# Kernel tuning notes

Hardware: AMD Instinct MI355X
Metric: run time of the kernel (lower is better)

## Reference

```python
import jax, jax.numpy as jnp
import numpy as np

B, T, C = 2, 2048, 1024
H, GAMMA = 16, 8
D = C // H
SCALE = 1.0 / np.sqrt(D).astype(np.float32)


def setup_inputs() -> dict:
    key = jax.random.key(0)
    ks = jax.random.split(key, 6)
    w = 0.02
    return {
        'x': jax.random.normal(ks[0], (B, T, C), dtype=jnp.float32),
        'Wq': jax.random.normal(ks[1], (C, 2 * C), dtype=jnp.float32) * w,
        'Wk': jax.random.normal(ks[2], (C, 2 * C), dtype=jnp.float32) * w,
        'Wv': jax.random.normal(ks[3], (C, C), dtype=jnp.float32) * w,
        'Wo': jax.random.normal(ks[4], (C, C), dtype=jnp.float32) * w,
        'theta_offset': jax.random.normal(ks[5], (H,), dtype=jnp.float32) * 0.1,
    }


def _heads(t):
    # (B, T, C) -> (B, H, T, D)
    return t.reshape(B, T, H, D).transpose(0, 2, 1, 3)


def reference(x, Wq, Wk, Wv, Wo, theta_offset):
    q_raw = x @ Wq                      # (B, T, 2C)
    k_raw = x @ Wk                      # (B, T, 2C)
    v = _heads(x @ Wv)                  # (B, H, T, D)

    q_amp, q_phase = jnp.split(q_raw, 2, axis=-1)
    k_amp, k_phase = jnp.split(k_raw, 2, axis=-1)
    q_amp = jax.nn.softplus(_heads(q_amp))
    q_phase = _heads(q_phase)
    k_amp = jax.nn.softplus(_heads(k_amp))
    k_phase = _heads(k_phase)

    q_real = q_amp * jnp.cos(q_phase)
    q_imag = q_amp * jnp.sin(q_phase)
    k_real = k_amp * jnp.cos(k_phase)
    k_imag = k_amp * jnp.sin(k_phase)

    scores = (jnp.einsum('bhtd,bhsd->bhts', q_real, k_real)
              + jnp.einsum('bhtd,bhsd->bhts', q_imag, k_imag)) * SCALE

    # theta gating (active since T > GAMMA)
    cycle_ids = jnp.arange(T, dtype=jnp.float32) / GAMMA
    cycle_dist = cycle_ids[None, :] - cycle_ids[:, None]        # (T, T)
    theta_gate = jnp.cos(theta_offset[:, None, None] * cycle_dist)  # (H, T, T)
    scores = scores * theta_gate[None]

    causal = jnp.tril(jnp.ones((T, T), dtype=bool))
    scores = jnp.where(causal[None, None], scores, -jnp.inf)
    attn = jax.nn.softmax(scores, axis=-1)

    out = jnp.einsum('bhts,bhsd->bhtd', attn, v)
    out = out.transpose(0, 2, 1, 3).reshape(B, T, C)
    return out @ Wo
```

## Files before the change

### kernel.cpp

```cpp
#include <hip/hip_runtime.h>
#include <hip/hip_bf16.h>
#include <math.h>

#define Bc 2
#define Tc 2048
#define Cc 1024
#define Hc 16
#define Dc 64

typedef __attribute__((ext_vector_type(8))) short short8;
typedef __attribute__((ext_vector_type(4))) float f32x4;

#define L2E 1.44269504088896f
#define SM_M 20.0f

__device__ __forceinline__ short f2bf(float x) {
    unsigned u = __float_as_uint(x);
    u += 0x7fff + ((u >> 16) & 1);
    return (short)(u >> 16);
}
__device__ __forceinline__ unsigned pack2bf_fast(float a, float b) {
    unsigned ua = __float_as_uint(a) + 0x8000u;
    unsigned ub = __float_as_uint(b) + 0x8000u;
    return __builtin_amdgcn_perm(ub, ua, 0x07060302);
}
__device__ __forceinline__ float softplus_fast(float a) {
    return fmaxf(a, 0.f) + __logf(1.f + __expf(-fabsf(a)));
}

template <int EPI>
__global__ __launch_bounds__(256) void gemm_bt_mfma(
    const short* __restrict__ A, const short* __restrict__ Bt,
    float* __restrict__ Cf, short* __restrict__ Cb, short* __restrict__ Cb2,
    int M, int N, int K)
{
    __shared__ __attribute__((aligned(16))) short As[128 * 32];
    __shared__ __attribute__((aligned(16))) short Bs[128 * 32];

    const int tid = threadIdx.x;
    const int wave = tid >> 6, lane = tid & 63;
    const int quad = lane >> 4, c = lane & 15;
    const int wm = wave >> 1, wn = wave & 1;
    const int m0 = blockIdx.y * 128, n0 = blockIdx.x * 128;

    const int srow = lane >> 2;
    const int scol = (lane & 3) * 8;
    const short* Ag = A  + (size_t)(m0 + wave * 32 + srow) * K + scol;
    const short* Bg = Bt + (size_t)(n0 + wave * 32 + srow) * K + scol;
    short* AsW = As + (wave * 32) * 32;
    short* BsW = Bs + (wave * 32) * 32;

    f32x4 acc[4][4];
#pragma unroll
    for (int i = 0; i < 4; ++i)
#pragma unroll
        for (int j = 0; j < 4; ++j)
            acc[i][j] = (f32x4){0.f, 0.f, 0.f, 0.f};

    for (int k0 = 0; k0 < K; k0 += 32) {
        __syncthreads();
#pragma unroll
        for (int i = 0; i < 2; ++i) {
            __builtin_amdgcn_global_load_lds(
                (const __attribute__((address_space(1))) void*)(Ag + k0 + (size_t)i * 16 * K),
                (__attribute__((address_space(3))) void*)(AsW + i * 16 * 32), 16, 0, 0);
            __builtin_amdgcn_global_load_lds(
                (const __attribute__((address_space(1))) void*)(Bg + k0 + (size_t)i * 16 * K),
                (__attribute__((address_space(3))) void*)(BsW + i * 16 * 32), 16, 0, 0);
        }
        __syncthreads();

        short8 af[4], bf[4];
#pragma unroll
        for (int mt = 0; mt < 4; ++mt)
            af[mt] = *(const short8*)&As[(wm * 64 + mt * 16 + c) * 32 + quad * 8];
#pragma unroll
        for (int nt = 0; nt < 4; ++nt)
            bf[nt] = *(const short8*)&Bs[(wn * 64 + nt * 16 + c) * 32 + quad * 8];
#pragma unroll
        for (int mt = 0; mt < 4; ++mt)
#pragma unroll
            for (int nt = 0; nt < 4; ++nt)
                acc[mt][nt] = __builtin_amdgcn_mfma_f32_16x16x32_bf16(
                    af[mt], bf[nt], acc[mt][nt], 0, 0, 0);
    }

    if (EPI == 2) {
        const int g = n0 >> 7;
        const int isK = g >> 4;
        const int h = g & 15;
        const float scl = isK ? 1.f : 0.125f;
        short* dst = isK ? Cb2 : Cb;
#pragma unroll
        for (int mt = 0; mt < 4; ++mt) {
#pragma unroll
            for (int reg = 0; reg < 4; ++reg) {
                int m = m0 + wm * 64 + mt * 16 + quad * 4 + reg;
                int bb = m >> 11, tt = m & (Tc - 1);
                size_t base = (((size_t)bb * Hc + h) * Tc + tt) * 128;
#pragma unroll
                for (int nt = 0; nt < 2; ++nt) {
                    float amp = acc[mt][nt][reg];
                    float ph  = acc[mt][nt + 2][reg];
                    int d = wn * 32 + nt * 16 + c;
                    float sp = softplus_fast(amp) * scl;
                    float sn, cs;
                    __sincosf(ph, &sn, &cs);
                    dst[base + d]      = f2bf(sp * cs);
                    dst[base + d + 64] = f2bf(sp * sn);
                }
            }
        }
    } else {
#pragma unroll
        for (int mt = 0; mt < 4; ++mt) {
#pragma unroll
            for (int reg = 0; reg < 4; ++reg) {
                size_t row = m0 + wm * 64 + mt * 16 + quad * 4 + reg;
#pragma unroll
                for (int nt = 0; nt < 4; ++nt) {
                    size_t col = n0 + wn * 64 + nt * 16 + c;
                    if (EPI == 1) Cb[row * N + col] = f2bf(acc[mt][nt][reg]);
                    else          Cf[row * N + col] = acc[mt][nt][reg];
                }
            }
        }
    }
}

__global__ __launch_bounds__(256) void gemm_v2t(
    const short* __restrict__ A, const short* __restrict__ Bt,
    short* __restrict__ v2t)
{
    __shared__ __attribute__((aligned(16))) short As[128 * 32];
    __shared__ __attribute__((aligned(16))) short Bs[128 * 32];
    __shared__ __attribute__((aligned(16))) short tile[128 * 136];

    const int K = Cc;
    const int tid = threadIdx.x;
    const int wave = tid >> 6, lane = tid & 63;
    const int quad = lane >> 4, c = lane & 15;
    const int wm = wave >> 1, wn = wave & 1;
    const int m0 = blockIdx.y * 128, n0 = blockIdx.x * 128;

    const int srow = lane >> 2;
    const int scol = (lane & 3) * 8;
    const short* Ag = A  + (size_t)(m0 + wave * 32 + srow) * K + scol;
    const short* Bg = Bt + (size_t)(n0 + wave * 32 + srow) * K + scol;
    short* AsW = As + (wave * 32) * 32;
    short* BsW = Bs + (wave * 32) * 32;

    f32x4 acc[4][4];
#pragma unroll
    for (int i = 0; i < 4; ++i)
#pragma unroll
        for (int j = 0; j < 4; ++j)
            acc[i][j] = (f32x4){0.f, 0.f, 0.f, 0.f};

    for (int k0 = 0; k0 < K; k0 += 32) {
        __syncthreads();
#pragma unroll
        for (int i = 0; i < 2; ++i) {
            __builtin_amdgcn_global_load_lds(
                (const __attribute__((address_space(1))) void*)(Ag + k0 + (size_t)i * 16 * K),
                (__attribute__((address_space(3))) void*)(AsW + i * 16 * 32), 16, 0, 0);
            __builtin_amdgcn_global_load_lds(
                (const __attribute__((address_space(1))) void*)(Bg + k0 + (size_t)i * 16 * K),
                (__attribute__((address_space(3))) void*)(BsW + i * 16 * 32), 16, 0, 0);
        }
        __syncthreads();

        short8 af[4], bf[4];
#pragma unroll
        for (int mt = 0; mt < 4; ++mt)
            af[mt] = *(const short8*)&As[(wm * 64 + mt * 16 + c) * 32 + quad * 8];
#pragma unroll
        for (int nt = 0; nt < 4; ++nt)
            bf[nt] = *(const short8*)&Bs[(wn * 64 + nt * 16 + c) * 32 + quad * 8];
#pragma unroll
        for (int mt = 0; mt < 4; ++mt)
#pragma unroll
            for (int nt = 0; nt < 4; ++nt)
                acc[mt][nt] = __builtin_amdgcn_mfma_f32_16x16x32_bf16(
                    af[mt], bf[nt], acc[mt][nt], 0, 0, 0);
    }

#pragma unroll
    for (int mt = 0; mt < 4; ++mt)
#pragma unroll
        for (int reg = 0; reg < 4; ++reg) {
            int tl = wm * 64 + mt * 16 + quad * 4 + reg;
#pragma unroll
            for (int nt = 0; nt < 4; ++nt)
                tile[(wn * 64 + nt * 16 + c) * 136 + tl] = f2bf(acc[mt][nt][reg]);
        }
    __syncthreads();

    const int b = m0 >> 11, tl0 = m0 & (Tc - 1);
#pragma unroll
    for (int i = 0; i < 8; ++i) {
        int n = i * 16 + (tid >> 4);
        int t8 = (tid & 15) * 8;
        int ng = n0 + n, h = ng >> 6, d = ng & 63;
        *(short8*)&v2t[(((size_t)b * Hc + h) * Dc + d) * Tc + tl0 + t8] =
            *(const short8*)&tile[n * 136 + t8];
    }
}

__global__ __launch_bounds__(256) void xconv(const float* __restrict__ x,
                                             short* __restrict__ xb)
{
    int idx = blockIdx.x * 256 + threadIdx.x;
    float4 v = *(const float4*)&x[(size_t)idx * 4];
    short4 o = {f2bf(v.x), f2bf(v.y), f2bf(v.z), f2bf(v.w)};
    *(short4*)&xb[(size_t)idx * 4] = o;
}

__global__ __launch_bounds__(256) void wtrans_qk(const float* __restrict__ Wq,
                                                 const float* __restrict__ Wk,
                                                 short* __restrict__ Bt)
{
    __shared__ short tile[64][80];
    const int n0 = blockIdx.x * 64, k0 = blockIdx.y * 64;
    const int half = blockIdx.z;
    const float* W = half ? Wk : Wq;
    const int tid = threadIdx.x;
#pragma unroll
    for (int i = 0; i < 4; ++i) {
        int e = i * 256 + tid;
        int k = e >> 4, n4 = (e & 15) * 4;
        float4 v = *(const float4*)&W[(size_t)(k0 + k) * 2048 + n0 + n4];
        tile[k][n4]     = f2bf(v.x);
        tile[k][n4 + 1] = f2bf(v.y);
        tile[k][n4 + 2] = f2bf(v.z);
        tile[k][n4 + 3] = f2bf(v.w);
    }
    __syncthreads();
#pragma unroll
    for (int i = 0; i < 16; ++i) {
        int e = i * 256 + tid;
        int n = e >> 6, k = e & 63;
        int ng = n0 + n;
        int sub = ng >> 10, hh = (ng >> 6) & 15, dd = ng & 63;
        int r = (half * 16 + hh) * 128 + (dd >> 5) * 64 + sub * 32 + (dd & 31);
        Bt[(size_t)r * Cc + k0 + k] = tile[k][n];
    }
}

__global__ __launch_bounds__(256) void wtrans2(const float* __restrict__ Wv,
                                               const float* __restrict__ Wo,
                                               short* __restrict__ WtBase)
{
    __shared__ short tile[64][80];
    const int n0 = blockIdx.x * 64, k0 = blockIdx.y * 64;
    const float* W = blockIdx.z ? Wo : Wv;
    short* Wt = WtBase + (size_t)blockIdx.z * Cc * Cc;
    const int tid = threadIdx.x;
#pragma unroll
    for (int i = 0; i < 4; ++i) {
        int e = i * 256 + tid;
        int k = e >> 4, n4 = (e & 15) * 4;
        float4 v = *(const float4*)&W[(size_t)(k0 + k) * Cc + n0 + n4];
        tile[k][n4]     = f2bf(v.x);
        tile[k][n4 + 1] = f2bf(v.y);
        tile[k][n4 + 2] = f2bf(v.z);
        tile[k][n4 + 3] = f2bf(v.w);
    }
    __syncthreads();
#pragma unroll
    for (int i = 0; i < 16; ++i) {
        int e = i * 256 + tid;
        int n = e >> 6, k = e & 63;
        Wt[(size_t)(n0 + n) * Cc + k0 + k] = tile[k][n];
    }
}

__global__ __launch_bounds__(512, 4) void moire_attn5(
    const short* __restrict__ q2, const short* __restrict__ k2,
    const short* __restrict__ v2t, const float* __restrict__ theta,
    short* __restrict__ att)
{
    __shared__ __attribute__((aligned(16))) short Ks[2][64 * 128];
    __shared__ __attribute__((aligned(16))) short Vt[2][64 * 64];
    __shared__ __attribute__((aligned(16))) short Ps[8][16 * 64];

    const int tid = threadIdx.x;
    const int wave = tid >> 6, lane = tid & 63;
    const int quad = lane >> 4, c = lane & 15;
    const int tx = wave >> 2, wq = wave & 3;
    const int p = blockIdx.x, h = blockIdx.y, b = blockIdx.z;
    const int qx = tx ? (31 - p) : p;
    const int q0 = qx * 64;
    const float th = theta[h];

    const short* k2b = k2 + (size_t)(b * Hc + h) * Tc * 128;
    const short* v2b = v2t + (size_t)(b * Hc + h) * Dc * Tc;

    short8 qf[4];
    const short* qp = q2 + ((size_t)(b * Hc + h) * Tc + q0 + wq * 16 + c) * 128;
#pragma unroll
    for (int i = 0; i < 4; ++i)
        qf[i] = *(const short8*)(qp + i * 32 + quad * 8);

    const int t_l = wq * 16 + c;
    float x0 = th * 0.125f * (float)(q0 + t_l);
    float cb = __cosf(x0), sb = -__sinf(x0);
    float cOff[4][4], sOff[4][4];
#pragma unroll
    for (int mt = 0; mt < 4; ++mt)
#pragma unroll
        for (int reg = 0; reg < 4; ++reg) {
            float a = th * 0.125f * (float)(mt * 16 + quad * 4 + reg);
            cOff[mt][reg] = __cosf(a) * L2E;
            sOff[mt][reg] = __sinf(a) * L2E;
        }
    const float cD = __cosf(8.f * th), sD = __sinf(8.f * th);

    f32x4 oacc[4];
    float lsum = 0.f;
#pragma unroll
    for (int nt = 0; nt < 4; ++nt)
        oacc[nt] = (f32x4){0.f, 0.f, 0.f, 0.f};

    auto stage = [&](int jts) {
        short* KsB = &Ks[jts & 1][0];
        short* VtB = &Vt[jts & 1][0];
        const int s0 = jts * 64;
#pragma unroll
        for (int i = 0; i < 2; ++i) {
            int ch = i * 512 + tid;
            int row = ch >> 4, j = ch & 15;
            const short* src = k2b + (size_t)(s0 + row) * 128 + ((j ^ (row & 15)) << 3);
            __builtin_amdgcn_global_load_lds(
                (const __attribute__((address_space(1))) void*)src,
                (__attribute__((address_space(3))) void*)(KsB + (i * 512 + wave * 64) * 8),
                16, 0, 0);
        }
        {
            int ch = tid;
            int row = ch >> 3, j = ch & 7;
            const short* src = v2b + (size_t)row * Tc + s0 + ((j ^ (row & 7)) << 3);
            __builtin_amdgcn_global_load_lds(
                (const __attribute__((address_space(1))) void*)src,
                (__attribute__((address_space(3))) void*)(VtB + (wave * 64) * 8),
                16, 0, 0);
        }
    };

    stage(0);
    const int jtEnd = 31 - p;
    for (int jt = 0; jt <= jtEnd; ++jt) {
        __syncthreads();
        if (jt < jtEnd) stage(jt + 1);

        if (jt <= qx) {
            const short* KsB = &Ks[jt & 1][0];
            const short* VtB = &Vt[jt & 1][0];
            const bool diag = (jt == qx);

            f32x4 s_acc[4];
#pragma unroll
            for (int mt = 0; mt < 4; ++mt) {
                f32x4 a = {0.f, 0.f, 0.f, 0.f};
#pragma unroll
                for (int kk = 0; kk < 4; ++kk) {
                    short8 kf = *(const short8*)&KsB[(mt * 16 + c) * 128 +
                                                     (((kk * 4 + quad) ^ c) << 3)];
                    a = __builtin_amdgcn_mfma_f32_16x16x32_bf16(kf, qf[kk], a, 0, 0, 0);
                }
                s_acc[mt] = a;
            }

#pragma unroll
            for (int mt = 0; mt < 4; ++mt) {
                float pv[4];
#pragma unroll
                for (int reg = 0; reg < 4; ++reg) {
                    float g2 = cb * cOff[mt][reg] - sb * sOff[mt][reg];
                    float arg = fmaf(s_acc[mt][reg], g2, -SM_M * L2E);
                    if (diag && (mt * 16 + quad * 4 + reg) > t_l) arg = -1e30f;
                    pv[reg] = exp2f(arg);
                }
                lsum += (pv[0] + pv[1]) + (pv[2] + pv[3]);
                uint2 pk = {pack2bf_fast(pv[0], pv[1]), pack2bf_fast(pv[2], pv[3])};
                int slot = ((mt * 2 + (quad >> 1)) ^ (c & 7));
                *(uint2*)&Ps[wave][c * 64 + slot * 8 + (quad & 1) * 4] = pk;
            }

            short8 pf[2];
#pragma unroll
            for (int kk = 0; kk < 2; ++kk)
                pf[kk] = *(const short8*)&Ps[wave][c * 64 +
                             (((kk * 4 + quad) ^ (c & 7)) << 3)];
#pragma unroll
            for (int nt = 0; nt < 4; ++nt)
#pragma unroll
                for (int kk = 0; kk < 2; ++kk) {
                    short8 vf = *(const short8*)&VtB[(nt * 16 + c) * 64 +
                                 (((kk * 4 + quad) ^ (c & 7)) << 3)];
                    oacc[nt] = __builtin_amdgcn_mfma_f32_16x16x32_bf16(
                        pf[kk], vf, oacc[nt], 0, 0, 0);
                }

            float ncb = cb * cD - sb * sD;
            sb = sb * cD + cb * sD;
            cb = ncb;
        }
    }

    float l = lsum;
    l += __shfl_xor(l, 16);
    l += __shfl_xor(l, 32);
    float il = 1.f / l;
    float ilr[4];
#pragma unroll
    for (int reg = 0; reg < 4; ++reg)
        ilr[reg] = __shfl(il, quad * 4 + reg);
#pragma unroll
    for (int reg = 0; reg < 4; ++reg) {
        int t_g = q0 + wq * 16 + quad * 4 + reg;
#pragma unroll
        for (int nt = 0; nt < 4; ++nt)
            att[(size_t)(b * Tc + t_g) * Cc + h * Dc + nt * 16 + c] =
                f2bf(oacc[nt][reg] * ilr[reg]);
    }
}

extern "C" void kernel_launch(void* const* d_in, const int* in_sizes, int n_in,
                              void* d_out, int out_size, void* d_ws, size_t ws_size,
                              hipStream_t stream)
{
    const float* x     = (const float*)d_in[0];
    const float* Wq    = (const float*)d_in[1];
    const float* Wk    = (const float*)d_in[2];
    const float* Wv    = (const float*)d_in[3];
    const float* Wo    = (const float*)d_in[4];
    const float* theta = (const float*)d_in[5];
    float* out = (float*)d_out;

    const int M = Bc * Tc;
    char* ws = (char*)d_ws;
    const size_t MB = 1 << 20;
    short* xb   = (short*)(ws);
    short* Bqk  = (short*)(ws + 8 * MB);
    short* Wvt  = (short*)(ws + 16 * MB);
    short* Wot  = (short*)(ws + 18 * MB);
    short* v2t  = (short*)(ws + 28 * MB);
    short* attb = (short*)(ws + 36 * MB);
    short* q2   = (short*)(ws + 44 * MB);
    short* k2   = (short*)d_out;

    xconv<<<(size_t)M * Cc / 1024, 256, 0, stream>>>(x, xb);
    wtrans_qk<<<dim3(2048 / 64, Cc / 64, 2), 256, 0, stream>>>(Wq, Wk, Bqk);
    wtrans2<<<dim3(Cc / 64, Cc / 64, 2), 256, 0, stream>>>(Wv, Wo, Wvt);

    gemm_bt_mfma<2><<<dim3(4096 / 128, M / 128), 256, 0, stream>>>(
        xb, Bqk, nullptr, q2, k2, M, 4096, Cc);
    gemm_v2t<<<dim3(Cc / 128, M / 128), 256, 0, stream>>>(xb, Wvt, v2t);

    moire_attn5<<<dim3(16, Hc, Bc), 512, 0, stream>>>(q2, k2, v2t, theta, attb);

    gemm_bt_mfma<0><<<dim3(Cc / 128, M / 128), 256, 0, stream>>>(
        attb, Wot, out, nullptr, nullptr, M, Cc, Cc);
}
```

Before: 263.7 us.

## Balance attention waves by splitting late query tile's KV range across both wave groups

Previously, within each block the four waves handling the early query tile sat idle once their tile finished, while the other four processed the late tile's full KV range. Now the early-tile waves, once done, switch to the late tile and take half of each KV block's columns. Their partial outputs and row sums are merged through shared memory at the end. This is meant to remove the intra-block load imbalance, at the cost of extra registers for a second accumulator, smaller MFMA chunks per wave, and an extra reduction pass.

```diff
diff --git a/kernel.cpp b/kernel.cpp
--- a/kernel.cpp
+++ b/kernel.cpp
@@ -275,7 +275,7 @@
     }
 }
 
-__global__ __launch_bounds__(512, 4) void moire_attn5(
+__global__ __launch_bounds__(512, 4) void moire_attn6(
     const short* __restrict__ q2, const short* __restrict__ k2,
     const short* __restrict__ v2t, const float* __restrict__ theta,
     short* __restrict__ att)
@@ -287,24 +287,31 @@
     const int tid = threadIdx.x;
     const int wave = tid >> 6, lane = tid & 63;
     const int quad = lane >> 4, c = lane & 15;
-    const int tx = wave >> 2, wq = wave & 3;
+    const int g = wave & 3;
+    const bool isU = wave >= 4;
     const int p = blockIdx.x, h = blockIdx.y, b = blockIdx.z;
-    const int qx = tx ? (31 - p) : p;
-    const int q0 = qx * 64;
+    const int pA = p, pB = 31 - p;
+    const int q0A = pA * 64, q0B = pB * 64;
     const float th = theta[h];
+    const int t_l = g * 16 + c;
 
     const short* k2b = k2 + (size_t)(b * Hc + h) * Tc * 128;
     const short* v2b = v2t + (size_t)(b * Hc + h) * Dc * Tc;
 
     short8 qf[4];
-    const short* qp = q2 + ((size_t)(b * Hc + h) * Tc + q0 + wq * 16 + c) * 128;
-#pragma unroll
-    for (int i = 0; i < 4; ++i)
-        qf[i] = *(const short8*)(qp + i * 32 + quad * 8);
-
-    const int t_l = wq * 16 + c;
-    float x0 = th * 0.125f * (float)(q0 + t_l);
-    float cb = __cosf(x0), sb = -__sinf(x0);
+    {
+        int q0 = isU ? q0A : q0B;
+        const short* qp = q2 + ((size_t)(b * Hc + h) * Tc + q0 + t_l) * 128;
+#pragma unroll
+        for (int i = 0; i < 4; ++i)
+            qf[i] = *(const short8*)(qp + i * 32 + quad * 8);
+    }
+
+    float cb, sb;
+    {
+        float x0 = th * 0.125f * (float)((isU ? q0A : q0B) + t_l);
+        cb = __cosf(x0); sb = -__sinf(x0);
+    }
     float cOff[4][4], sOff[4][4];
 #pragma unroll
     for (int mt = 0; mt < 4; ++mt)
@@ -317,10 +324,13 @@
     const float cD = __cosf(8.f * th), sD = __sinf(8.f * th);
 
     f32x4 oacc[4];
-    float lsum = 0.f;
-#pragma unroll
-    for (int nt = 0; nt < 4; ++nt)
-        oacc[nt] = (f32x4){0.f, 0.f, 0.f, 0.f};
+    f32x4 oacc2[4];
+    float lsum = 0.f, lsum2 = 0.f;
+#pragma unroll
+    for (int nt = 0; nt < 4; ++nt) {
+        oacc[nt]  = (f32x4){0.f, 0.f, 0.f, 0.f};
+        oacc2[nt] = (f32x4){0.f, 0.f, 0.f, 0.f};
+    }
 
     auto stage = [&](int jts) {
         short* KsB = &Ks[jts & 1][0];
@@ -347,82 +357,133 @@
         }
     };
 
+    auto doHalf = [&](int hh, bool diag, f32x4* oa, float& ls,
+                      const short* KsB, const short* VtB) {
+        f32x4 s_acc[2];
+#pragma unroll
+        for (int m2 = 0; m2 < 2; ++m2) {
+            int mt = hh * 2 + m2;
+            f32x4 a = {0.f, 0.f, 0.f, 0.f};
+#pragma unroll
+            for (int kk = 0; kk < 4; ++kk) {
+                short8 kf = *(const short8*)&KsB[(mt * 16 + c) * 128 +
+                                                 (((kk * 4 + quad) ^ c) << 3)];
+                a = __builtin_amdgcn_mfma_f32_16x16x32_bf16(kf, qf[kk], a, 0, 0, 0);
+            }
+            s_acc[m2] = a;
+        }
+#pragma unroll
+        for (int m2 = 0; m2 < 2; ++m2) {
+            int mt = hh * 2 + m2;
+            float pv[4];
+#pragma unroll
+            for (int reg = 0; reg < 4; ++reg) {
+                float g2 = cb * cOff[mt][reg] - sb * sOff[mt][reg];
+                float arg = fmaf(s_acc[m2][reg], g2, -SM_M * L2E);
+                if (diag && (mt * 16 + quad * 4 + reg) > t_l) arg = -1e30f;
+                pv[reg] = exp2f(arg);
+            }
+            ls += (pv[0] + pv[1]) + (pv[2] + pv[3]);
+            uint2 pk = {pack2bf_fast(pv[0], pv[1]), pack2bf_fast(pv[2], pv[3])};
+            int slot = ((mt * 2 + (quad >> 1)) ^ (c & 7));
+            *(uint2*)&Ps[wave][c * 64 + slot * 8 + (quad & 1) * 4] = pk;
+        }
+        short8 pf = *(const short8*)&Ps[wave][c * 64 +
+                         (((hh * 4 + quad) ^ (c & 7)) << 3)];
+#pragma unroll
+        for (int nt = 0; nt < 4; ++nt) {
+            short8 vf = *(const short8*)&VtB[(nt * 16 + c) * 64 +
+                         (((hh * 4 + quad) ^ (c & 7)) << 3)];
+            oa[nt] = __builtin_amdgcn_mfma_f32_16x16x32_bf16(pf, vf, oa[nt], 0, 0, 0);
+        }
+    };
+
     stage(0);
-    const int jtEnd = 31 - p;
-    for (int jt = 0; jt <= jtEnd; ++jt) {
+    for (int jt = 0; jt <= pB; ++jt) {
         __syncthreads();
-        if (jt < jtEnd) stage(jt + 1);
-
-        if (jt <= qx) {
-            const short* KsB = &Ks[jt & 1][0];
-            const short* VtB = &Vt[jt & 1][0];
-            const bool diag = (jt == qx);
-
-            f32x4 s_acc[4];
-#pragma unroll
-            for (int mt = 0; mt < 4; ++mt) {
-                f32x4 a = {0.f, 0.f, 0.f, 0.f};
-#pragma unroll
-                for (int kk = 0; kk < 4; ++kk) {
-                    short8 kf = *(const short8*)&KsB[(mt * 16 + c) * 128 +
-                                                     (((kk * 4 + quad) ^ c) << 3)];
-                    a = __builtin_amdgcn_mfma_f32_16x16x32_bf16(kf, qf[kk], a, 0, 0, 0);
-                }
-                s_acc[mt] = a;
+        if (jt < pB) stage(jt + 1);
+        const short* KsB = &Ks[jt & 1][0];
+        const short* VtB = &Vt[jt & 1][0];
+
+        if (isU && jt == pA + 1) {
+            const short* qp = q2 + ((size_t)(b * Hc + h) * Tc + q0B + t_l) * 128;
+#pragma unroll
+            for (int i = 0; i < 4; ++i)
+                qf[i] = *(const short8*)(qp + i * 32 + quad * 8);
+            float xx = th * 0.125f * (float)(jt * 64 - q0B - t_l);
+            cb = __cosf(xx); sb = __sinf(xx);
+        }
+
+        if (jt <= pA) {
+            bool diag = isU && (jt == pA);
+            doHalf(0, diag, oacc, lsum, KsB, VtB);
+            doHalf(1, diag, oacc, lsum, KsB, VtB);
+        } else {
+            bool diag = (jt == pB);
+            if (!isU) doHalf(0, diag, oacc,  lsum,  KsB, VtB);
+            else      doHalf(1, diag, oacc2, lsum2, KsB, VtB);
+        }
+
+        float ncb = cb * cD - sb * sD;
+        sb = sb * cD + cb * sD;
+        cb = ncb;
+    }
+
+    __syncthreads();
+    float* Ox = (float*)&Ks[0][0];
+    float* Lx = (float*)&Vt[0][0];
+
+    if (isU) {
+        float l2 = lsum2;
+        l2 += __shfl_xor(l2, 16);
+        l2 += __shfl_xor(l2, 32);
+        Lx[g * 16 + c] = l2;
+#pragma unroll
+        for (int nt = 0; nt < 4; ++nt)
+#pragma unroll
+            for (int reg = 0; reg < 4; ++reg)
+                Ox[g * 1040 + (quad * 4 + reg) * 65 + nt * 16 + c] = oacc2[nt][reg];
+    }
+    __syncthreads();
+
+    if (!isU) {
+        float l = lsum;
+        l += __shfl_xor(l, 16);
+        l += __shfl_xor(l, 32);
+        l += Lx[g * 16 + c];
+        float il = 1.f / l;
+        float ilr[4];
+#pragma unroll
+        for (int reg = 0; reg < 4; ++reg)
+            ilr[reg] = __shfl(il, quad * 4 + reg);
+#pragma unroll
+        for (int reg = 0; reg < 4; ++reg) {
+            int t_g = q0B + g * 16 + quad * 4 + reg;
+#pragma unroll
+            for (int nt = 0; nt < 4; ++nt) {
+                float o = oacc[nt][reg] +
+                          Ox[g * 1040 + (quad * 4 + reg) * 65 + nt * 16 + c];
+                att[(size_t)(b * Tc + t_g) * Cc + h * Dc + nt * 16 + c] =
+                    f2bf(o * ilr[reg]);
             }
-
-#pragma unroll
-            for (int mt = 0; mt < 4; ++mt) {
-                float pv[4];
-#pragma unroll
-                for (int reg = 0; reg < 4; ++reg) {
-                    float g2 = cb * cOff[mt][reg] - sb * sOff[mt][reg];
-                    float arg = fmaf(s_acc[mt][reg], g2, -SM_M * L2E);
-                    if (diag && (mt * 16 + quad * 4 + reg) > t_l) arg = -1e30f;
-                    pv[reg] = exp2f(arg);
-                }
-                lsum += (pv[0] + pv[1]) + (pv[2] + pv[3]);
-                uint2 pk = {pack2bf_fast(pv[0], pv[1]), pack2bf_fast(pv[2], pv[3])};
-                int slot = ((mt * 2 + (quad >> 1)) ^ (c & 7));
-                *(uint2*)&Ps[wave][c * 64 + slot * 8 + (quad & 1) * 4] = pk;
-            }
-
-            short8 pf[2];
-#pragma unroll
-            for (int kk = 0; kk < 2; ++kk)
-                pf[kk] = *(const short8*)&Ps[wave][c * 64 +
-                             (((kk * 4 + quad) ^ (c & 7)) << 3)];
+        }
+    } else {
+        float l = lsum;
+        l += __shfl_xor(l, 16);
+        l += __shfl_xor(l, 32);
+        float il = 1.f / l;
+        float ilr[4];
+#pragma unroll
+        for (int reg = 0; reg < 4; ++reg)
+            ilr[reg] = __shfl(il, quad * 4 + reg);
+#pragma unroll
+        for (int reg = 0; reg < 4; ++reg) {
+            int t_g = q0A + g * 16 + quad * 4 + reg;
 #pragma unroll
             for (int nt = 0; nt < 4; ++nt)
-#pragma unroll
-                for (int kk = 0; kk < 2; ++kk) {
-                    short8 vf = *(const short8*)&VtB[(nt * 16 + c) * 64 +
-                                 (((kk * 4 + quad) ^ (c & 7)) << 3)];
-                    oacc[nt] = __builtin_amdgcn_mfma_f32_16x16x32_bf16(
-                        pf[kk], vf, oacc[nt], 0, 0, 0);
-                }
-
-            float ncb = cb * cD - sb * sD;
-            sb = sb * cD + cb * sD;
-            cb = ncb;
-        }
-    }
-
-    float l = lsum;
-    l += __shfl_xor(l, 16);
-    l += __shfl_xor(l, 32);
-    float il = 1.f / l;
-    float ilr[4];
-#pragma unroll
-    for (int reg = 0; reg < 4; ++reg)
-        ilr[reg] = __shfl(il, quad * 4 + reg);
-#pragma unroll
-    for (int reg = 0; reg < 4; ++reg) {
-        int t_g = q0 + wq * 16 + quad * 4 + reg;
-#pragma unroll
-        for (int nt = 0; nt < 4; ++nt)
-            att[(size_t)(b * Tc + t_g) * Cc + h * Dc + nt * 16 + c] =
-                f2bf(oacc[nt][reg] * ilr[reg]);
+                att[(size_t)(b * Tc + t_g) * Cc + h * Dc + nt * 16 + c] =
+                    f2bf(oacc[nt][reg] * ilr[reg]);
+        }
     }
 }
 
@@ -458,7 +519,7 @@
         xb, Bqk, nullptr, q2, k2, M, 4096, Cc);
     gemm_v2t<<<dim3(Cc / 128, M / 128), 256, 0, stream>>>(xb, Wvt, v2t);
 
-    moire_attn5<<<dim3(16, Hc, Bc), 512, 0, stream>>>(q2, k2, v2t, theta, attb);
+    moire_attn6<<<dim3(16, Hc, Bc), 512, 0, stream>>>(q2, k2, v2t, theta, attb);
 
     gemm_bt_mfma<0><<<dim3(Cc / 128, M / 128), 256, 0, stream>>>(
         attb, Wot, out, nullptr, nullptr, M, Cc, Cc);
```

Result: slower. 355.7 us (+34.9%).
